# Kernel optimization log

Measured on AMD Instinct MI355X. Metric: run time of the kernel, lower is better.

The kernel has to match this reference:

```python
import jax, jax.numpy as jnp
import numpy as np

B, L = 4, 2048
D_MODEL, D_INNER, D_STATE, DT_RANK, D_CONV = 1024, 2048, 16, 64, 4


def setup_inputs() -> dict:
    key = jax.random.key(0)
    ks = jax.random.split(key, 10)
    s = lambda k, shape, sc: jax.random.normal(k, shape, dtype=jnp.float32) * sc
    return {
        "x": s(ks[0], (B, L, D_MODEL), 1.0),
        "W_in": s(ks[1], (2 * D_INNER, D_MODEL), D_MODEL ** -0.5),
        "conv_w": s(ks[2], (D_INNER, D_CONV), D_CONV ** -0.5),
        "conv_b": s(ks[3], (D_INNER,), 0.02),
        "A_log": jnp.log(jnp.arange(1, D_STATE + 1, dtype=jnp.float32)),
        "D": jnp.ones((D_INNER,), dtype=jnp.float32),
        "W_x": s(ks[4], (DT_RANK + 2 * D_STATE, D_INNER), D_INNER ** -0.5),
        "W_dt": s(ks[5], (D_INNER, DT_RANK), DT_RANK ** -0.5),
        "b_dt": s(ks[6], (D_INNER,), 0.02) - 4.0,  # softplus -> small positive dt
        "W_out": s(ks[7], (D_MODEL, D_INNER), D_INNER ** -0.5),
    }


def reference(x, W_in, conv_w, conv_b, A_log, D, W_x, W_dt, b_dt, W_out):
    Bb, Ll, _ = x.shape
    # input projection, split into ssm branch and gate branch
    xz = x @ W_in.T                       # (B, L, 2*Di)
    xr, z = jnp.split(xz, 2, axis=-1)     # (B, L, Di) each
    # depthwise causal conv1d (torch pads both sides then slices [:L])
    xc = jax.lax.conv_general_dilated(
        xr.transpose(0, 2, 1),            # (B, Di, L)
        conv_w[:, None, :],               # (Di, 1, K)
        window_strides=(1,),
        padding=[(D_CONV - 1, 0)],
        dimension_numbers=("NCH", "OIH", "NCH"),
        feature_group_count=D_INNER,
    ) + conv_b[None, :, None]
    xs = jax.nn.silu(xc.transpose(0, 2, 1))  # (B, L, Di)
    # input-dependent dt, B, C
    x_dbl = xs @ W_x.T                        # (B, L, dt_rank + 2*S)
    dt_r, b_sel, c_sel = jnp.split(x_dbl, [DT_RANK, DT_RANK + D_STATE], axis=-1)
    dt = jax.nn.softplus(dt_r @ W_dt.T + b_dt)  # (B, L, Di)
    a_diag = -jnp.exp(A_log)                    # (S,)

    def step(h, inp):
        dt_t, b_t, c_t, x_t = inp                       # (B,Di),(B,S),(B,S),(B,Di)
        a_bar = jnp.exp(dt_t[:, :, None] * a_diag)      # (B, Di, S)
        h = a_bar * h + (dt_t * x_t)[:, :, None] * b_t[:, None, :]
        y = jnp.einsum("bds,bs->bd", h, c_t) + D * x_t
        return h, y

    h0 = jnp.zeros((Bb, D_INNER, D_STATE), dtype=x.dtype)
    _, ys = jax.lax.scan(
        step, h0,
        (dt.transpose(1, 0, 2), b_sel.transpose(1, 0, 2),
         c_sel.transpose(1, 0, 2), xs.transpose(1, 0, 2)),
    )
    y = ys.transpose(1, 0, 2)                           # (B, L, Di)
    return (y * jax.nn.silu(z)) @ W_out.T               # (B, L, d_model)
```

## Files before the change

kernel.cpp:

```cpp
#include <hip/hip_runtime.h>
#include <math.h>

typedef unsigned short u16;
typedef unsigned int u32;

constexpr int Bb = 4, Ll = 2048, DM = 1024, DI = 2048, DS = 16, DTR = 64, KC = 4;
constexpr int M = Bb * Ll;
constexpr int NPAD = 128;
constexpr int NCHUNK = 32;
constexpr int LC = Ll / NCHUNK;
constexpr int LDXZ = 4096;

__device__ __forceinline__ float b2f(u16 u) {
    return __uint_as_float(((u32)u) << 16);
}
__device__ __forceinline__ u16 f2b(float f) {
    u32 x = __float_as_uint(f);
    u32 r = (x + 0x7fffu + ((x >> 16) & 1u)) >> 16;
    return (u16)r;
}

typedef __attribute__((ext_vector_type(8))) short short8;
typedef __attribute__((ext_vector_type(4))) short short4v;
typedef __attribute__((ext_vector_type(4))) float floatx4;

__device__ __forceinline__ void gload16(const u16* g, u16* l) {
    __builtin_amdgcn_global_load_lds(
        (const __attribute__((address_space(1))) void*)g,
        (__attribute__((address_space(3))) void*)l,
        16, 0, 0);
}

__device__ __forceinline__ void pow_tree(float a, float* aa) {
    float a2 = a * a, a4 = a2 * a2, a8 = a4 * a4;
    aa[0] = a;        aa[1] = a2;       aa[2] = a * a2;   aa[3] = a4;
    aa[4] = a * a4;   aa[5] = a2 * a4;  aa[6] = aa[2] * a4; aa[7] = a8;
    aa[8] = a * a8;   aa[9] = a2 * a8;  aa[10] = aa[2] * a8; aa[11] = a4 * a8;
    aa[12] = aa[4] * a8; aa[13] = aa[5] * a8; aa[14] = aa[6] * a8; aa[15] = a8 * a8;
}

template<int OUTM>
__global__ __launch_bounds__(512, 2) void gemm256(
    const u16* __restrict__ A, const u16* __restrict__ Bm,
    void* __restrict__ Cv,
    int K, int lda, int ldb, int ldc)
{
    __shared__ alignas(16) u16 ldsA[4][256 * 32];
    __shared__ alignas(16) u16 ldsB[4][256 * 32];

    const int lane = threadIdx.x & 63;
    const int wave = threadIdx.x >> 6;
    const int wr = wave >> 2;
    const int wc = wave & 3;
    const int m0 = blockIdx.y * 256;
    const int n0 = blockIdx.x * 256;

    const int lrow = lane >> 2;
    const int skc  = (((lane & 3) + (lane >> 3)) & 3) * 8;
    const u16* pA = A  + (size_t)(m0 + wave * 32 + lrow) * lda + skc;
    const u16* pB = Bm + (size_t)(n0 + wave * 32 + lrow) * ldb + skc;
    const int ldst = wave * 1024;

    const int r16 = lane & 15;
    const int quad = lane >> 4;
    const int slot = (quad + 4 - ((r16 >> 1) & 3)) & 3;
    const int aoff = (wr * 128 + r16) * 32 + slot * 8;
    const int boff = (wc * 64  + r16) * 32 + slot * 8;

    const int NT = K >> 5;

    floatx4 acc[8][4] = {};

#pragma unroll
    for (int t = 0; t < 3; ++t) {
        gload16(pA + t * 32,            &ldsA[t][ldst]);
        gload16(pA + t * 32 + 16 * lda, &ldsA[t][ldst + 512]);
        gload16(pB + t * 32,            &ldsB[t][ldst]);
        gload16(pB + t * 32 + 16 * ldb, &ldsB[t][ldst + 512]);
    }
    asm volatile("s_waitcnt vmcnt(8)" ::: "memory");
    __builtin_amdgcn_sched_barrier(0);
    __builtin_amdgcn_s_barrier();

    for (int t = 0; t < NT; ++t) {
        const u16* la = &ldsA[t & 3][aoff];
        const u16* lb = &ldsB[t & 3][boff];
        short8 af[8], bf[4];

#pragma unroll
        for (int i = 0; i < 4; ++i) af[i] = *(const short8*)(la + i * 512);
#pragma unroll
        for (int j = 0; j < 4; ++j) bf[j] = *(const short8*)(lb + j * 512);
        if (t + 3 < NT) {
            const u16* s = pA + (t + 3) * 32;
            u16* d = &ldsA[(t + 3) & 3][ldst];
            gload16(s, d);
            gload16(s + 16 * lda, d + 512);
        }
        __builtin_amdgcn_sched_barrier(0);
        __builtin_amdgcn_s_barrier();
        asm volatile("s_waitcnt lgkmcnt(0)" ::: "memory");
        __builtin_amdgcn_sched_barrier(0);
        __builtin_amdgcn_s_setprio(1);
#pragma unroll
        for (int i = 0; i < 4; ++i)
#pragma unroll
            for (int j = 0; j < 4; ++j)
                acc[i][j] = __builtin_amdgcn_mfma_f32_16x16x32_bf16(
                    af[i], bf[j], acc[i][j], 0, 0, 0);
        __builtin_amdgcn_s_setprio(0);
        __builtin_amdgcn_sched_barrier(0);
        __builtin_amdgcn_s_barrier();

#pragma unroll
        for (int i = 4; i < 8; ++i) af[i] = *(const short8*)(la + i * 512);
        if (t + 3 < NT) {
            const u16* s = pB + (t + 3) * 32;
            u16* d = &ldsB[(t + 3) & 3][ldst];
            gload16(s, d);
            gload16(s + 16 * ldb, d + 512);
        }
        __builtin_amdgcn_sched_barrier(0);
        __builtin_amdgcn_s_barrier();
        asm volatile("s_waitcnt lgkmcnt(0)" ::: "memory");
        __builtin_amdgcn_sched_barrier(0);
        __builtin_amdgcn_s_setprio(1);
#pragma unroll
        for (int i = 4; i < 8; ++i)
#pragma unroll
            for (int j = 0; j < 4; ++j)
                acc[i][j] = __builtin_amdgcn_mfma_f32_16x16x32_bf16(
                    af[i], bf[j], acc[i][j], 0, 0, 0);
        __builtin_amdgcn_s_setprio(0);
        if (t + 3 < NT)      asm volatile("s_waitcnt vmcnt(8)" ::: "memory");
        else if (t + 2 < NT) asm volatile("s_waitcnt vmcnt(4)" ::: "memory");
        else if (t + 1 < NT) asm volatile("s_waitcnt vmcnt(0)" ::: "memory");
        __builtin_amdgcn_sched_barrier(0);
        __builtin_amdgcn_s_barrier();
    }

    const int mw = m0 + wr * 128;
    const int nw = n0 + wc * 64;
    const int rb = quad * 4;
#pragma unroll
    for (int i = 0; i < 8; ++i) {
#pragma unroll
        for (int j = 0; j < 4; ++j) {
            const int n = nw + j * 16 + r16;
#pragma unroll
            for (int r = 0; r < 4; ++r) {
                const int m = mw + i * 16 + rb + r;
                float v = acc[i][j][r];
                if (OUTM == 1)
                    ((float*)Cv)[(size_t)m * ldc + n] = v;
                else
                    ((u16*)Cv)[(size_t)m * ldc + n] = f2b(v);
            }
        }
    }
}

template<int OUTM>
__global__ __launch_bounds__(512, 4) void gemm256n128(
    const u16* __restrict__ A, const u16* __restrict__ Bm,
    void* __restrict__ Cv,
    int K, int lda, int ldb, int ldc)
{
    __shared__ alignas(16) u16 ldsA[3][256 * 32];
    __shared__ alignas(16) u16 ldsB[3][128 * 32];

    const int lane = threadIdx.x & 63;
    const int wave = threadIdx.x >> 6;
    const int wr = wave >> 1;
    const int wc = wave & 1;
    const int m0 = blockIdx.y * 256;
    const int n0 = blockIdx.x * 128;

    const int lrow = lane >> 2;
    const int skc  = (((lane & 3) + (lane >> 3)) & 3) * 8;
    const u16* pA = A  + (size_t)(m0 + wave * 32 + lrow) * lda + skc;
    const u16* pB = Bm + (size_t)(n0 + wave * 16 + lrow) * ldb + skc;
    const int ldstA = wave * 1024;
    const int ldstB = wave * 512;

    const int r16 = lane & 15;
    const int quad = lane >> 4;
    const int slot = (quad + 4 - ((r16 >> 1) & 3)) & 3;
    const int aoff = (wr * 64 + r16) * 32 + slot * 8;
    const int boff = (wc * 64 + r16) * 32 + slot * 8;

    const int NT = K >> 5;

    floatx4 acc[4][4] = {};

#pragma unroll
    for (int t = 0; t < 2; ++t) {
        gload16(pA + t * 32,            &ldsA[t][ldstA]);
        gload16(pA + t * 32 + 16 * lda, &ldsA[t][ldstA + 512]);
        gload16(pB + t * 32,            &ldsB[t][ldstB]);
    }
    asm volatile("s_waitcnt vmcnt(3)" ::: "memory");
    __builtin_amdgcn_sched_barrier(0);
    __builtin_amdgcn_s_barrier();

    int bc = 0, bs = 2;
    for (int t = 0; t < NT; ++t) {
        const u16* la = &ldsA[bc][aoff];
        const u16* lb = &ldsB[bc][boff];
        short8 af[4], bf[4];
#pragma unroll
        for (int i = 0; i < 4; ++i) af[i] = *(const short8*)(la + i * 512);
#pragma unroll
        for (int j = 0; j < 4; ++j) bf[j] = *(const short8*)(lb + j * 512);
        if (t + 2 < NT) {
            const u16* sa = pA + (t + 2) * 32;
            u16* da = &ldsA[bs][ldstA];
            gload16(sa, da);
            gload16(sa + 16 * lda, da + 512);
            gload16(pB + (t + 2) * 32, &ldsB[bs][ldstB]);
        }
        __builtin_amdgcn_sched_barrier(0);
        __builtin_amdgcn_s_barrier();
        asm volatile("s_waitcnt lgkmcnt(0)" ::: "memory");
        __builtin_amdgcn_sched_barrier(0);
        __builtin_amdgcn_s_setprio(1);
#pragma unroll
        for (int i = 0; i < 4; ++i)
#pragma unroll
            for (int j = 0; j < 4; ++j)
                acc[i][j] = __builtin_amdgcn_mfma_f32_16x16x32_bf16(
                    af[i], bf[j], acc[i][j], 0, 0, 0);
        __builtin_amdgcn_s_setprio(0);
        if (t + 2 < NT)      asm volatile("s_waitcnt vmcnt(3)" ::: "memory");
        else if (t + 1 < NT) asm volatile("s_waitcnt vmcnt(0)" ::: "memory");
        __builtin_amdgcn_sched_barrier(0);
        __builtin_amdgcn_s_barrier();
        bc = (bc == 2) ? 0 : bc + 1;
        bs = (bs == 2) ? 0 : bs + 1;
    }

    const int mw = m0 + wr * 64;
    const int nw = n0 + wc * 64;
    const int rb = quad * 4;
#pragma unroll
    for (int i = 0; i < 4; ++i) {
#pragma unroll
        for (int j = 0; j < 4; ++j) {
            const int n = nw + j * 16 + r16;
#pragma unroll
            for (int r = 0; r < 4; ++r) {
                const int m = mw + i * 16 + rb + r;
                float v = acc[i][j][r];
                if (OUTM == 1)
                    ((float*)Cv)[(size_t)m * ldc + n] = v;
                else
                    ((u16*)Cv)[(size_t)m * ldc + n] = f2b(v);
            }
        }
    }
}

template<int OUTM>
__global__ __launch_bounds__(256) void gemm_bt(
    const u16* __restrict__ A, const u16* __restrict__ Bm,
    void* __restrict__ Cv, const float* __restrict__ bias,
    int K, int lda, int ldb, int ldc)
{
    __shared__ alignas(16) u16 ldsA[128 * 32];
    __shared__ alignas(16) u16 ldsB[128 * 32];

    const int lane = threadIdx.x & 63;
    const int wave = threadIdx.x >> 6;
    const int wr = wave >> 1, wc = wave & 1;
    const int m0 = blockIdx.y * 128;
    const int n0 = blockIdx.x * 128;
    const int koff = (OUTM == 4) ? blockIdx.z * K : 0;

    const int srow = wave * 32 + (lane >> 2);
    const int skc  = (((lane & 3) + (lane >> 3)) & 3) * 8;
    const u16* Ag = A + (size_t)(m0 + srow) * lda + skc + koff;
    const u16* Bg = Bm + (size_t)(n0 + srow) * ldb + skc + koff;
    u16* lA = &ldsA[wave * 1024];
    u16* lB = &ldsB[wave * 1024];

    const int r16 = lane & 15;
    const int quad = lane >> 4;
    const int slot = (quad + 4 - ((r16 >> 1) & 3)) & 3;
    const u16* arow = &ldsA[(wr * 64 + r16) * 32 + slot * 8];
    const u16* brow = &ldsB[(wc * 64 + r16) * 32 + slot * 8];

    floatx4 acc[4][4] = {};

    for (int k0 = 0; k0 < K; k0 += 32) {
        gload16(Ag + k0,                    lA);
        gload16(Ag + k0 + (size_t)16 * lda, lA + 512);
        gload16(Bg + k0,                    lB);
        gload16(Bg + k0 + (size_t)16 * ldb, lB + 512);
        __syncthreads();

        short8 af[4], bf[4];
#pragma unroll
        for (int i = 0; i < 4; i++) af[i] = *(const short8*)(arow + i * 16 * 32);
#pragma unroll
        for (int j = 0; j < 4; j++) bf[j] = *(const short8*)(brow + j * 16 * 32);
#pragma unroll
        for (int i = 0; i < 4; i++)
#pragma unroll
            for (int j = 0; j < 4; j++)
                acc[i][j] = __builtin_amdgcn_mfma_f32_16x16x32_bf16(
                    af[i], bf[j], acc[i][j], 0, 0, 0);
        __syncthreads();
    }

    const int mw = m0 + wr * 64;
    const int nw = n0 + wc * 64;
    const int rb = quad * 4;
#pragma unroll
    for (int i = 0; i < 4; i++) {
#pragma unroll
        for (int j = 0; j < 4; j++) {
            const int n = nw + j * 16 + r16;
#pragma unroll
            for (int r = 0; r < 4; r++) {
                const int m = mw + i * 16 + rb + r;
                float v = acc[i][j][r];
                if (OUTM == 2) {
                    v += bias[n];
                    v = (v > 20.f) ? v : log1pf(__expf(v));
                }
                if (OUTM == 4)
                    ((float*)Cv)[((size_t)blockIdx.z * M + m) * ldc + n] = v;
                else if (OUTM == 1)
                    ((float*)Cv)[(size_t)m * ldc + n] = v;
                else
                    ((u16*)Cv)[(size_t)m * ldc + n] = f2b(v);
            }
        }
    }
}

__global__ __launch_bounds__(256) void redk_gemm3(
    const float* __restrict__ part, u16* __restrict__ xdbl,
    float* __restrict__ bcf)
{
    const int t = blockIdx.x * 256 + threadIdx.x;
    const int n4 = (t & 31) * 4;
    const int m = t >> 5;
    const size_t stride = (size_t)M * NPAD;
    const float* p = part + (size_t)m * NPAD + n4;
    floatx4 acc = *(const floatx4*)(p)
                + *(const floatx4*)(p + stride)
                + *(const floatx4*)(p + 2 * stride)
                + *(const floatx4*)(p + 3 * stride);
    short4v ob;
#pragma unroll
    for (int j = 0; j < 4; j++) ob[j] = (short)f2b(acc[j]);
    *(short4v*)(xdbl + (size_t)m * NPAD + n4) = ob;
    if (n4 >= 64 && n4 < 96)
        *(floatx4*)(bcf + (size_t)m * 32 + (n4 - 64)) = acc;
}

__global__ __launch_bounds__(256) void prep_all(
    const float* __restrict__ x, const float* __restrict__ W_in,
    const float* __restrict__ W_x, const float* __restrict__ W_dt,
    const float* __restrict__ W_out,
    u16* __restrict__ xbf, u16* __restrict__ wibf, u16* __restrict__ wxp,
    u16* __restrict__ wdtb, u16* __restrict__ woutb)
{
    constexpr int N0 = M * DM;
    constexpr int N1 = 2 * DI * DM;
    constexpr int N2 = NPAD * DI;
    constexpr int N3 = DI * DTR;
    int idx = blockIdx.x * blockDim.x + threadIdx.x;
    if (idx < N0) {
        xbf[idx] = f2b(x[idx]);
        return;
    }
    idx -= N0;
    if (idx < N1) {
        wibf[idx] = f2b(W_in[idx]);
    } else if (idx < N1 + N2) {
        int i = idx - N1;
        int r = i >> 11, c = i & 2047;
        wxp[i] = (r < 96) ? f2b(W_x[r * 2048 + c]) : (u16)0;
    } else if (idx < N1 + N2 + N3) {
        int i = idx - N1 - N2;
        wdtb[i] = f2b(W_dt[i]);
    } else {
        int i = idx - N1 - N2 - N3;
        woutb[i] = f2b(W_out[i]);
    }
}

__global__ __launch_bounds__(256) void conv_silu(
    const u16* __restrict__ xz, const float* __restrict__ conv_w,
    const float* __restrict__ conv_b, u16* __restrict__ xs)
{
    const int m = blockIdx.x;
    const int d0 = threadIdx.x * 8;
    const int l = m & (Ll - 1);

    float acc[8];
    {
        floatx4 cb0 = *(const floatx4*)(conv_b + d0);
        floatx4 cb1 = *(const floatx4*)(conv_b + d0 + 4);
#pragma unroll
        for (int j = 0; j < 4; j++) { acc[j] = cb0[j]; acc[4 + j] = cb1[j]; }
    }
    float w[8][KC];
#pragma unroll
    for (int jd = 0; jd < 8; jd++) {
        floatx4 wv = *(const floatx4*)(conv_w + (d0 + jd) * KC);
#pragma unroll
        for (int k = 0; k < KC; k++) w[jd][k] = wv[k];
    }
#pragma unroll
    for (int k = 0; k < KC; k++) {
        int li = l - (KC - 1) + k;
        if (li >= 0) {
            short8 xv = *(const short8*)(xz + (size_t)(m - (KC - 1) + k) * LDXZ + d0);
#pragma unroll
            for (int jd = 0; jd < 8; jd++)
                acc[jd] += b2f((u16)xv[jd]) * w[jd][k];
        }
    }
    short8 o;
#pragma unroll
    for (int jd = 0; jd < 8; jd++) {
        float s = acc[jd] / (1.f + __expf(-acc[jd]));
        o[jd] = (short)f2b(s);
    }
    *(short8*)(xs + (size_t)m * DI + d0) = o;
}

__global__ __launch_bounds__(256) void scan_p1(
    const u16* __restrict__ xzdt, const u16* __restrict__ xs,
    const float* __restrict__ bcf, const float* __restrict__ A_log,
    float* __restrict__ scr_h, float* __restrict__ sdt_g)
{
    __shared__ alignas(16) float bcs[LC * 32];

    const int d = blockIdx.x * 256 + threadIdx.x;
    const int b = blockIdx.y;
    const int c = blockIdx.z;
    const int m0 = b * Ll + c * LC;

    {
        const float* bc_g = bcf + (size_t)m0 * 32;
#pragma unroll
        for (int j = 0; j < 2; j++) {
            int idx = j * 1024 + threadIdx.x * 4;
            *(floatx4*)(bcs + idx) = *(const floatx4*)(bc_g + idx);
        }
    }

    const float ad0 = -__expf(A_log[0]);
    float adl[DS];
    bool fast = true;
#pragma unroll
    for (int s = 0; s < DS; s++) {
        float av = -__expf(A_log[s]);
        adl[s] = av;
        float kr = (float)(s + 1);
        if (fabsf(av / ad0 - kr) > 1e-4f * kr) fast = false;
    }

    const u16* dt_p = xzdt + (size_t)m0 * LDXZ + d;
    const u16* xs_p = xs + (size_t)m0 * DI + d;

    float h[DS] = {};
    float sdt = 0.f;

    __syncthreads();

    u16 dt_c = dt_p[0],     xs_c = xs_p[0];
    u16 dt_1 = dt_p[LDXZ],  xs_1 = xs_p[DI];

    if (fast) {
        for (int l = 0; l < LC; l++) {
            u16 dt_2 = dt_p[2 * LDXZ];
            u16 xs_2 = xs_p[2 * DI];
            const float* bl = bcs + l * 32;
            floatx4 B0 = *(const floatx4*)(bl);
            floatx4 B1 = *(const floatx4*)(bl + 4);
            floatx4 B2 = *(const floatx4*)(bl + 8);
            floatx4 B3 = *(const floatx4*)(bl + 12);

            float dtv = b2f(dt_c);
            float xv  = b2f(xs_c);
            float bx = dtv * xv;
            sdt += dtv;
            float aa[DS];
            pow_tree(__expf(dtv * ad0), aa);
#pragma unroll
            for (int s = 0; s < DS; s++) {
                float Bv = (s < 4) ? B0[s] : (s < 8) ? B1[s - 4]
                         : (s < 12) ? B2[s - 8] : B3[s - 12];
                h[s] = aa[s] * h[s] + bx * Bv;
            }
            dt_c = dt_1; dt_1 = dt_2; xs_c = xs_1; xs_1 = xs_2;
            dt_p += LDXZ; xs_p += DI;
        }
    } else {
        for (int l = 0; l < LC; l++) {
            u16 dt_2 = dt_p[2 * LDXZ];
            u16 xs_2 = xs_p[2 * DI];
            const float* bl = bcs + l * 32;
            floatx4 B0 = *(const floatx4*)(bl);
            floatx4 B1 = *(const floatx4*)(bl + 4);
            floatx4 B2 = *(const floatx4*)(bl + 8);
            floatx4 B3 = *(const floatx4*)(bl + 12);

            float dtv = b2f(dt_c);
            float xv  = b2f(xs_c);
            float bx = dtv * xv;
            sdt += dtv;
#pragma unroll
            for (int s = 0; s < DS; s++) {
                float Bv = (s < 4) ? B0[s] : (s < 8) ? B1[s - 4]
                         : (s < 12) ? B2[s - 8] : B3[s - 12];
                float a = __expf(dtv * adl[s]);
                h[s] = a * h[s] + bx * Bv;
            }
            dt_c = dt_1; dt_1 = dt_2; xs_c = xs_1; xs_1 = xs_2;
            dt_p += LDXZ; xs_p += DI;
        }
    }

    const size_t base = ((size_t)(b * NCHUNK + c) * DI + d) * DS;
#pragma unroll
    for (int s = 0; s < DS; s += 4) {
        floatx4 hv = {h[s], h[s+1], h[s+2], h[s+3]};
        *(floatx4*)(scr_h + base + s) = hv;
    }
    sdt_g[(size_t)(b * NCHUNK + c) * DI + d] = sdt;
}

__global__ __launch_bounds__(256) void scan_p2(
    float* __restrict__ scr_h, const float* __restrict__ sdt_g,
    const float* __restrict__ A_log)
{
    const int t = blockIdx.x * 256 + threadIdx.x;
    const int s = t & 15;
    const int d = (t >> 4) & (DI - 1);
    const int b = t >> 15;
    const float adl = -__expf(A_log[s]);

    float he[NCHUNK], P[NCHUNK];
#pragma unroll
    for (int c = 0; c < NCHUNK; c++) {
        const size_t base = ((size_t)(b * NCHUNK + c) * DI + d) * DS + s;
        he[c] = scr_h[base];
        P[c] = adl * sdt_g[(size_t)(b * NCHUNK + c) * DI + d];
    }
#pragma unroll
    for (int c = 0; c < NCHUNK; c++) P[c] = __expf(P[c]);
    float hin = 0.f;
#pragma unroll
    for (int c = 0; c < NCHUNK; c++) {
        const size_t base = ((size_t)(b * NCHUNK + c) * DI + d) * DS + s;
        scr_h[base] = hin;
        hin = P[c] * hin + he[c];
    }
}

__global__ __launch_bounds__(256) void scan_p3(
    const u16* __restrict__ xz, const u16* xs, const float* __restrict__ bcf,
    const float* __restrict__ scr_hin, const float* __restrict__ A_log,
    const float* __restrict__ Dvec, u16* yg)
{
    __shared__ alignas(16) float bcs[LC * 32];

    const int d = blockIdx.x * 256 + threadIdx.x;
    const int b = blockIdx.y;
    const int c = blockIdx.z;
    const int m0 = b * Ll + c * LC;

    {
        const float* bc_g = bcf + (size_t)m0 * 32;
#pragma unroll
        for (int j = 0; j < 2; j++) {
            int idx = j * 1024 + threadIdx.x * 4;
            *(floatx4*)(bcs + idx) = *(const floatx4*)(bc_g + idx);
        }
    }

    const float ad0 = -__expf(A_log[0]);
    float adl[DS];
    bool fast = true;
#pragma unroll
    for (int s = 0; s < DS; s++) {
        float av = -__expf(A_log[s]);
        adl[s] = av;
        float kr = (float)(s + 1);
        if (fabsf(av / ad0 - kr) > 1e-4f * kr) fast = false;
    }
    const float Dd = Dvec[d];

    const u16* dt_p = xz + (size_t)m0 * LDXZ + d;
    const u16* z_p  = xz + (size_t)m0 * LDXZ + 2048 + d;
    const u16* xs_p = xs + (size_t)m0 * DI + d;
    u16* yg_p = yg + (size_t)m0 * DI + d;

    float h[DS];
    const size_t base = ((size_t)(b * NCHUNK + c) * DI + d) * DS;
#pragma unroll
    for (int s = 0; s < DS; s += 4) {
        floatx4 hv = *(const floatx4*)(scr_hin + base + s);
        h[s] = hv[0]; h[s+1] = hv[1]; h[s+2] = hv[2]; h[s+3] = hv[3];
    }

    __syncthreads();

    u16 dt_c = dt_p[0],    dt_1 = dt_p[LDXZ];
    u16 xs_c = xs_p[0],    xs_1 = xs_p[DI];
    u16 z_c  = z_p[0],     z_1  = z_p[LDXZ];

    for (int l = 0; l < LC; l++) {
        u16 dt_2 = dt_p[2 * LDXZ];
        u16 xs_2 = xs_p[2 * DI];
        u16 z_2  = z_p[2 * LDXZ];
        const float* bl = bcs + l * 32;
        floatx4 Bq[4], Cq[4];
#pragma unroll
        for (int q = 0; q < 4; q++) {
            Bq[q] = *(const floatx4*)(bl + q * 4);
            Cq[q] = *(const floatx4*)(bl + 16 + q * 4);
        }

        float dtv = b2f(dt_c);
        float xv  = b2f(xs_c);
        float bx = dtv * xv;
        float aa[DS];
        if (fast) {
            pow_tree(__expf(dtv * ad0), aa);
        } else {
#pragma unroll
            for (int s = 0; s < DS; s++) aa[s] = __expf(dtv * adl[s]);
        }
        float y0 = 0.f, y1 = 0.f, y2 = 0.f, y3 = 0.f;
#pragma unroll
        for (int q = 0; q < 4; q++) {
#pragma unroll
            for (int j = 0; j < 4; j++) {
                int s = q * 4 + j;
                h[s] = aa[s] * h[s] + bx * Bq[q][j];
            }
        }
#pragma unroll
        for (int j = 0; j < 4; j++) {
            y0 += h[j] * Cq[0][j];
            y1 += h[4 + j] * Cq[1][j];
            y2 += h[8 + j] * Cq[2][j];
            y3 += h[12 + j] * Cq[3][j];
        }
        float yt = ((y0 + y1) + (y2 + y3)) + Dd * xv;
        float zv = b2f(z_c);
        float g = zv / (1.f + __expf(-zv));
        yg_p[0] = f2b(yt * g);

        dt_c = dt_1; dt_1 = dt_2;
        xs_c = xs_1; xs_1 = xs_2;
        z_c  = z_1;  z_1  = z_2;
        dt_p += LDXZ; xs_p += DI; z_p += LDXZ; yg_p += DI;
    }
}

extern "C" void kernel_launch(void* const* d_in, const int* in_sizes, int n_in,
                              void* d_out, int out_size, void* d_ws, size_t ws_size,
                              hipStream_t stream)
{
    const float* x      = (const float*)d_in[0];
    const float* W_in   = (const float*)d_in[1];
    const float* conv_w = (const float*)d_in[2];
    const float* conv_b = (const float*)d_in[3];
    const float* A_log  = (const float*)d_in[4];
    const float* Dvec   = (const float*)d_in[5];
    const float* W_x    = (const float*)d_in[6];
    const float* W_dt   = (const float*)d_in[7];
    const float* b_dt   = (const float*)d_in[8];
    const float* W_out  = (const float*)d_in[9];

    u16* ws = (u16*)d_ws;
    u16* xz    = ws;                 ws += (size_t)M * LDXZ;
    u16* xs    = ws;                 ws += (size_t)M * DI;
    u16* xbf   = ws;                 ws += (size_t)M * DM;
    u16* wibf  = ws;                 ws += (size_t)2 * DI * DM;
    u16* wxp   = ws;                 ws += (size_t)NPAD * DI;
    u16* wdtb  = ws;                 ws += (size_t)DI * DTR;
    u16* woutb = ws;                 ws += (size_t)DM * DI;
    u16* xdbl  = ws;                 ws += (size_t)M * NPAD;
    u16* yg    = xs;
    float* part  = (float*)xbf;
    float* scr_h = (float*)xbf;
    float* bcf   = (float*)wibf;
    float* sdt_g = bcf + (size_t)M * 32;

    {
        constexpr int NTOT = M * DM + 2 * DI * DM + NPAD * DI + DI * DTR + DM * DI;
        prep_all<<<NTOT / 256, 256, 0, stream>>>(
            x, W_in, W_x, W_dt, W_out, xbf, wibf, wxp, wdtb, woutb);
    }

    gemm256<0><<<dim3(LDXZ / 256, M / 256), 512, 0, stream>>>(
        xbf, wibf, xz, DM, DM, DM, LDXZ);

    conv_silu<<<M, 256, 0, stream>>>(xz, conv_w, conv_b, xs);

    gemm_bt<4><<<dim3(1, M / 128, 4), 256, 0, stream>>>(
        xs, wxp, part, nullptr, DI / 4, DI, DI, NPAD);
    redk_gemm3<<<(M * 32) / 256, 256, 0, stream>>>(part, xdbl, bcf);

    gemm_bt<2><<<dim3(DI / 128, M / 128), 256, 0, stream>>>(
        xdbl, wdtb, xz, b_dt, DTR, NPAD, DTR, LDXZ);

    scan_p1<<<dim3(DI / 256, Bb, NCHUNK), 256, 0, stream>>>(
        xz, xs, bcf, A_log, scr_h, sdt_g);
    scan_p2<<<(Bb * DI * DS) / 256, 256, 0, stream>>>(scr_h, sdt_g, A_log);
    scan_p3<<<dim3(DI / 256, Bb, NCHUNK), 256, 0, stream>>>(
        xz, xs, bcf, scr_h, A_log, Dvec, yg);

    gemm256n128<1><<<dim3(DM / 128, M / 256), 512, 0, stream>>>(
        yg, woutb, d_out, DI, DI, DI, DM);
}
```

Baseline: 476.1 us.

## Add XCD-aware block swizzle to GEMMs, merge k-loop halves, shrink x_dbl reduction

```diff
diff --git a/kernel.cpp b/kernel.cpp
--- a/kernel.cpp
+++ b/kernel.cpp
@@ -39,6 +39,22 @@
     aa[12] = aa[4] * a8; aa[13] = aa[5] * a8; aa[14] = aa[6] * a8; aa[15] = a8 * a8;
 }
 
+template<int GX, int GY>
+__device__ __forceinline__ void xcd_swizzle(int& bx, int& by) {
+    const int bid = blockIdx.y * GX + blockIdx.x;
+    const int xcd = bid & 7;
+    const int i = bid >> 3;
+    const int c_local = i >> 5;
+    const int within = i & 31;
+    const int lx = within & 7, ly = within >> 3;
+    const int chunk = xcd + c_local * 8;
+    constexpr int CXN = GX / 8;
+    const int cx = chunk % CXN;
+    const int cy = chunk / CXN;
+    bx = cx * 8 + lx;
+    by = cy * 4 + ly;
+}
+
 template<int OUTM>
 __global__ __launch_bounds__(512, 2) void gemm256(
     const u16* __restrict__ A, const u16* __restrict__ Bm,
@@ -48,12 +64,15 @@
     __shared__ alignas(16) u16 ldsA[4][256 * 32];
     __shared__ alignas(16) u16 ldsB[4][256 * 32];
 
+    int bx, by;
+    xcd_swizzle<16, 32>(bx, by);
+
     const int lane = threadIdx.x & 63;
     const int wave = threadIdx.x >> 6;
     const int wr = wave >> 2;
     const int wc = wave & 3;
-    const int m0 = blockIdx.y * 256;
-    const int n0 = blockIdx.x * 256;
+    const int m0 = by * 256;
+    const int n0 = bx * 256;
 
     const int lrow = lane >> 2;
     const int skc  = (((lane & 3) + (lane >> 3)) & 3) * 8;
@@ -86,16 +105,19 @@
         const u16* la = &ldsA[t & 3][aoff];
         const u16* lb = &ldsB[t & 3][boff];
         short8 af[8], bf[4];
-
-#pragma unroll
-        for (int i = 0; i < 4; ++i) af[i] = *(const short8*)(la + i * 512);
+#pragma unroll
+        for (int i = 0; i < 8; ++i) af[i] = *(const short8*)(la + i * 512);
 #pragma unroll
         for (int j = 0; j < 4; ++j) bf[j] = *(const short8*)(lb + j * 512);
         if (t + 3 < NT) {
-            const u16* s = pA + (t + 3) * 32;
-            u16* d = &ldsA[(t + 3) & 3][ldst];
-            gload16(s, d);
-            gload16(s + 16 * lda, d + 512);
+            const u16* sA = pA + (t + 3) * 32;
+            const u16* sB = pB + (t + 3) * 32;
+            u16* dA = &ldsA[(t + 3) & 3][ldst];
+            u16* dB = &ldsB[(t + 3) & 3][ldst];
+            gload16(sA, dA);
+            gload16(sA + 16 * lda, dA + 512);
+            gload16(sB, dB);
+            gload16(sB + 16 * ldb, dB + 512);
         }
         __builtin_amdgcn_sched_barrier(0);
         __builtin_amdgcn_s_barrier();
@@ -103,30 +125,7 @@
         __builtin_amdgcn_sched_barrier(0);
         __builtin_amdgcn_s_setprio(1);
 #pragma unroll
-        for (int i = 0; i < 4; ++i)
-#pragma unroll
-            for (int j = 0; j < 4; ++j)
-                acc[i][j] = __builtin_amdgcn_mfma_f32_16x16x32_bf16(
-                    af[i], bf[j], acc[i][j], 0, 0, 0);
-        __builtin_amdgcn_s_setprio(0);
-        __builtin_amdgcn_sched_barrier(0);
-        __builtin_amdgcn_s_barrier();
-
-#pragma unroll
-        for (int i = 4; i < 8; ++i) af[i] = *(const short8*)(la + i * 512);
-        if (t + 3 < NT) {
-            const u16* s = pB + (t + 3) * 32;
-            u16* d = &ldsB[(t + 3) & 3][ldst];
-            gload16(s, d);
-            gload16(s + 16 * ldb, d + 512);
-        }
-        __builtin_amdgcn_sched_barrier(0);
-        __builtin_amdgcn_s_barrier();
-        asm volatile("s_waitcnt lgkmcnt(0)" ::: "memory");
-        __builtin_amdgcn_sched_barrier(0);
-        __builtin_amdgcn_s_setprio(1);
-#pragma unroll
-        for (int i = 4; i < 8; ++i)
+        for (int i = 0; i < 8; ++i)
 #pragma unroll
             for (int j = 0; j < 4; ++j)
                 acc[i][j] = __builtin_amdgcn_mfma_f32_16x16x32_bf16(
@@ -169,12 +168,15 @@
     __shared__ alignas(16) u16 ldsA[3][256 * 32];
     __shared__ alignas(16) u16 ldsB[3][128 * 32];
 
+    int bx, by;
+    xcd_swizzle<8, 32>(bx, by);
+
     const int lane = threadIdx.x & 63;
     const int wave = threadIdx.x >> 6;
     const int wr = wave >> 1;
     const int wc = wave & 1;
-    const int m0 = blockIdx.y * 256;
-    const int n0 = blockIdx.x * 128;
+    const int m0 = by * 256;
+    const int n0 = bx * 128;
 
     const int lrow = lane >> 2;
     const int skc  = (((lane & 3) + (lane >> 3)) & 3) * 8;
@@ -344,20 +346,23 @@
     float* __restrict__ bcf)
 {
     const int t = blockIdx.x * 256 + threadIdx.x;
-    const int n4 = (t & 31) * 4;
-    const int m = t >> 5;
+    const int c4 = t % 24;
+    const int m = t / 24;
+    const int n4 = c4 * 4;
     const size_t stride = (size_t)M * NPAD;
     const float* p = part + (size_t)m * NPAD + n4;
     floatx4 acc = *(const floatx4*)(p)
                 + *(const floatx4*)(p + stride)
                 + *(const floatx4*)(p + 2 * stride)
                 + *(const floatx4*)(p + 3 * stride);
-    short4v ob;
-#pragma unroll
-    for (int j = 0; j < 4; j++) ob[j] = (short)f2b(acc[j]);
-    *(short4v*)(xdbl + (size_t)m * NPAD + n4) = ob;
-    if (n4 >= 64 && n4 < 96)
+    if (n4 < 64) {
+        short4v ob;
+#pragma unroll
+        for (int j = 0; j < 4; j++) ob[j] = (short)f2b(acc[j]);
+        *(short4v*)(xdbl + (size_t)m * 64 + n4) = ob;
+    } else {
         *(floatx4*)(bcf + (size_t)m * 32 + (n4 - 64)) = acc;
+    }
 }
 
 __global__ __launch_bounds__(256) void prep_all(
@@ -709,10 +714,10 @@
 
     gemm_bt<4><<<dim3(1, M / 128, 4), 256, 0, stream>>>(
         xs, wxp, part, nullptr, DI / 4, DI, DI, NPAD);
-    redk_gemm3<<<(M * 32) / 256, 256, 0, stream>>>(part, xdbl, bcf);
+    redk_gemm3<<<(M * 24) / 256, 256, 0, stream>>>(part, xdbl, bcf);
 
     gemm_bt<2><<<dim3(DI / 128, M / 128), 256, 0, stream>>>(
-        xdbl, wdtb, xz, b_dt, DTR, NPAD, DTR, LDXZ);
+        xdbl, wdtb, xz, b_dt, DTR, 64, DTR, LDXZ);
 
     scan_p1<<<dim3(DI / 256, Bb, NCHUNK), 256, 0, stream>>>(
         xz, xs, bcf, A_log, scr_h, sdt_g);
```

After: 463.1 us. 1.03x faster.
